# Kernel optimization log

Measured on AMD Instinct MI355X. Metric: run time of the kernel, lower is better.

The kernel has to match this reference:

```python
import jax, jax.numpy as jnp
import numpy as np

GRID = 32


def setup_inputs() -> dict:
    key = jax.random.key(0)
    k1, k2, k3 = jax.random.split(key, 3)
    # points in [-0.5, 0.5] per the module's asserts
    x = jax.random.uniform(k1, (8, 3, 50000), minval=-0.5, maxval=0.5, dtype=jnp.float32)
    # prep = Conv2d(3, 16, kernel_size=1): weight [C,3], bias [C]
    W = jax.random.normal(k2, (16, 3), dtype=jnp.float32) * 0.1
    bias = jax.random.normal(k3, (16,), dtype=jnp.float32) * 0.1
    return {"x": x, "W": W, "bias": bias}


def reference(x, W, bias):
    G = GRID
    b, _, n = x.shape
    reshaped = (x + 0.5) * G - 0.5                      # [b,3,n]
    ind1 = jnp.clip(jnp.floor(reshaped), 0.0, G - 1)
    ind2 = jnp.clip(jnp.ceil(reshaped), 0.0, G - 1)
    # 8 corners, ordered (floor/ceil over x, then y, then z) to match original list
    corners = []
    for cx in (ind1, ind2):
        for cy in (ind1, ind2):
            for cz in (ind1, ind2):
                corners.append(jnp.stack([cx[:, 0], cy[:, 1], cz[:, 2]], axis=1))
    ind = jnp.stack(corners, axis=-1)                   # [b,3,n,8]
    res = reshaped[..., None] - ind                     # [b,3,n,8] residuals
    flat_idx = (ind[:, 0] * (G * G) + ind[:, 1] * G + ind[:, 2]).astype(jnp.int32)  # [b,n,8]
    flat_idx = jnp.clip(flat_idx, 0, G ** 3)            # mirrors indices.clamp_(0, G**3)
    dist = jnp.linalg.norm(res, axis=1)                 # [b,n,8]
    weight = (dist < 0.87).astype(res.dtype)            # [b,n,8] (detached in original)
    # prep: 1x1 conv over channel dim
    feat = jnp.einsum('bknp,ck->bcnp', res, W) + bias[None, :, None, None]  # [b,c,n,8]
    feat = feat * weight[:, None]                       # mask by ball weight
    c = feat.shape[1]
    feat_f = feat.reshape(b, c, n * 8)
    w_f = jnp.broadcast_to(weight[:, None], feat.shape).reshape(b, c, n * 8)
    i_f = flat_idx.reshape(b, n * 8)

    def scatter_one(f, w, idx):
        g = jnp.zeros((c, G ** 3), f.dtype).at[:, idx].add(f)
        cnt = jnp.zeros((c, G ** 3), f.dtype).at[:, idx].add(w)
        return g, cnt

    grid, count = jax.vmap(scatter_one)(feat_f, w_f, i_f)  # [b,c,G^3] each
    grid = grid / jnp.maximum(count, 1.0)
    return grid.reshape(b, c, G, G, G)
```

## Files before the change

kernel.cpp:

```cpp
#include <hip/hip_runtime.h>

#define G 32
#define G2 (G*G)
#define G3 (G*G*G)
#define NPTS 50000
#define NB 8
#define NC 16
#define NCHUNK_PER_B 49
#define NCHUNK (NB*NCHUNK_PER_B)
#define SUBCAP 1024

#define OFF_HIST    0
#define OFF_PAYLOAD 65536

__global__ __launch_bounds__(1024) void ge_bin(const float* __restrict__ x,
                                               int* __restrict__ hist,
                                               float4* __restrict__ payload) {
    __shared__ float4 sp[2048];
    __shared__ unsigned char spl[2048];
    __shared__ int h[G];
    __shared__ int offs[G + 1];

    const int tid = threadIdx.x;
    const int b   = blockIdx.y;
    const int c   = b * NCHUNK_PER_B + blockIdx.x;
    const int n   = blockIdx.x * 1024 + tid;
    const bool valid = n < NPTS;

    if (tid < G) h[tid] = 0;
    __syncthreads();

    float rx = 0.f, ry = 0.f, rz = 0.f, fr1 = 1.0f;
    int p1 = 0, p2 = 0, r1 = 0, r2 = 0;
    if (valid) {
        const float* xb = x + (size_t)b * 3 * NPTS;
        rx = (xb[n]          + 0.5f) * 32.0f - 0.5f;
        ry = (xb[NPTS + n]   + 0.5f) * 32.0f - 0.5f;
        rz = (xb[2*NPTS + n] + 0.5f) * 32.0f - 0.5f;
        p1 = (int)fminf(fmaxf(floorf(rx), 0.0f), 31.0f);
        p2 = (int)fminf(fmaxf(ceilf (rx), 0.0f), 31.0f);
        if (p1 == p2) {
            fr1 = 2.0f;
            r1 = atomicAdd(&h[p1], 1);
        } else {
            r1 = atomicAdd(&h[p1], 1);
            r2 = atomicAdd(&h[p2], 1);
        }
    }
    __syncthreads();

    if (tid == 0) {
        int run = 0;
        #pragma unroll
        for (int p = 0; p < G; ++p) { offs[p] = run; run += h[p]; }
        offs[G] = run;
    }
    __syncthreads();

    if (valid) {
        int e1 = offs[p1] + r1;
        sp[e1]  = make_float4(rx, ry, rz, fr1);
        spl[e1] = (unsigned char)p1;
        if (p1 != p2) {
            int e2 = offs[p2] + r2;
            sp[e2]  = make_float4(rx, ry, rz, 1.0f);
            spl[e2] = (unsigned char)p2;
        }
    }
    if (tid < G) hist[c * G + tid] = h[tid];
    __syncthreads();

    const int T = offs[G];
    float4* chunk_pl = payload + (size_t)c * G * SUBCAP;
    for (int e = tid; e < T; e += 1024) {
        int p = spl[e];
        chunk_pl[(size_t)p * SUBCAP + (e - offs[p])] = sp[e];
    }
}

__global__ __launch_bounds__(1024) void ge_accum(const float4* __restrict__ payload,
                                                 const int* __restrict__ hist,
                                                 const float* __restrict__ W,
                                                 const float* __restrict__ bias,
                                                 float* __restrict__ out) {
    __shared__ unsigned long long A[G2];
    const int tid = threadIdx.x;
    const int b = blockIdx.x >> 5;
    const int s = blockIdx.x & 31;
    const float fs = (float)s;

    A[tid] = 0ull;
    __syncthreads();

    const int wave = tid >> 6, lane = tid & 63;
    for (int blk = wave; blk < NCHUNK_PER_B; blk += 16) {
        const int cc  = b * NCHUNK_PER_B + blk;
        const int ec  = hist[cc * G + s];
        const float4* q = payload + ((size_t)cc * G + s) * SUBCAP;
        for (int i = lane; i < ec; i += 64) {
            float4 e = q[i];
            float dx = e.x - fs;
            float ry = e.y, rz = e.z;
            unsigned fri = (unsigned)e.w;

            float fy1 = fminf(fmaxf(floorf(ry), 0.0f), 31.0f);
            float fy2 = fminf(fmaxf(ceilf (ry), 0.0f), 31.0f);
            float fz1 = fminf(fmaxf(floorf(rz), 0.0f), 31.0f);
            float fz2 = fminf(fmaxf(ceilf (rz), 0.0f), 31.0f);
            float dy1 = ry - fy1, dy2 = ry - fy2;
            float dz1 = rz - fz1, dz2 = rz - fz2;

            unsigned ax  = (unsigned)((int)rintf(dx  * 2048.0f) + 2048) * fri;
            unsigned ay1 = (unsigned)((int)rintf(dy1 * 2048.0f) + 2048) * fri;
            unsigned ay2 = (unsigned)((int)rintf(dy2 * 2048.0f) + 2048) * fri;
            unsigned az1 = (unsigned)((int)rintf(dz1 * 2048.0f) + 2048) * fri;
            unsigned az2 = (unsigned)((int)rintf(dz2 * 2048.0f) + 2048) * fri;
            unsigned long long base = ((unsigned long long)fri << 57)
                                    | ((unsigned long long)ax  << 38);
            float dx2 = dx * dx;

            #pragma unroll
            for (int cy = 0; cy < 2; ++cy) {
                float iy = cy ? fy2 : fy1;
                float dy = cy ? dy2 : dy1;
                unsigned ay = cy ? ay2 : ay1;
                float dxy2 = dx2 + dy * dy;
                #pragma unroll
                for (int cz = 0; cz < 2; ++cz) {
                    float iz = cz ? fz2 : fz1;
                    float dz = cz ? dz2 : dz1;
                    float d2 = dxy2 + dz * dz;
                    if (d2 < 0.7569f) {
                        int cell = (int)iy * G + (int)iz;
                        unsigned az = cz ? az2 : az1;
                        atomicAdd(&A[cell],
                                  base | ((unsigned long long)ay << 19)
                                       | (unsigned long long)az);
                    }
                }
            }
        }
    }
    __syncthreads();

    const unsigned long long a = A[tid];
    const float cw = (float)(unsigned)(a >> 57);
    const float fxs = (float)(unsigned)((a >> 38) & 0x7FFFFull);
    const float fys = (float)(unsigned)((a >> 19) & 0x7FFFFull);
    const float fzs = (float)(unsigned)( a         & 0x7FFFFull);
    const float k = 1.0f / 2048.0f;
    const float sx = (fxs - 2048.0f * cw) * k;
    const float sy = (fys - 2048.0f * cw) * k;
    const float sz = (fzs - 2048.0f * cw) * k;
    const float inv = 1.0f / fmaxf(cw, 1.0f);

    float* ob = out + (size_t)b * NC * G3 + (size_t)s * G2 + tid;
    #pragma unroll
    for (int ch = 0; ch < NC; ++ch) {
        float v = W[ch * 3 + 0] * sx + W[ch * 3 + 1] * sy + W[ch * 3 + 2] * sz
                + cw * bias[ch];
        ob[(size_t)ch * G3] = v * inv;
    }
}

#define SEG 12288
#define QMAX SEG
__global__ __launch_bounds__(1024) void ge_fused(const float* __restrict__ x,
                                                 const float* __restrict__ W,
                                                 const float* __restrict__ bias,
                                                 float* __restrict__ out) {
    __shared__ float acc[G2][4];
    __shared__ int   q[QMAX];
    __shared__ int   qcount;
    const int b = blockIdx.x >> 5;
    const int s = blockIdx.x & 31;
    const float fs = (float)s;
    const int lane = threadIdx.x & 63;
    for (int i = threadIdx.x; i < G2 * 4; i += 1024) ((float*)acc)[i] = 0.0f;
    if (threadIdx.x == 0) qcount = 0;
    __syncthreads();
    const float* xb = x + (size_t)b * 3 * NPTS;
    for (int seg = 0; seg < NPTS; seg += SEG) {
        const int seg_end = (seg + SEG < NPTS) ? seg + SEG : NPTS;
        for (int base = seg; base < seg_end; base += 1024) {
            int n = base + threadIdx.x;
            bool pred = false; int tag = 0;
            if (n < seg_end) {
                float rx = (xb[n] + 0.5f) * 32.0f - 0.5f;
                int p1 = (int)fminf(fmaxf(floorf(rx), 0.0f), 31.0f);
                int p2 = (int)fminf(fmaxf(ceilf (rx), 0.0f), 31.0f);
                int reps = (p1 == s) + (p2 == s);
                pred = reps > 0;
                tag = n | (reps == 2 ? (int)0x80000000 : 0);
            }
            unsigned long long mask = __ballot(pred);
            int wcnt = __popcll(mask);
            if (wcnt) {
                int wbase = 0;
                if (lane == 0) wbase = atomicAdd(&qcount, wcnt);
                wbase = __shfl(wbase, 0);
                if (pred) q[wbase + __popcll(mask & ((1ULL << lane) - 1ULL))] = tag;
            }
        }
        __syncthreads();
        const int cnt = qcount;
        for (int i = threadIdx.x; i < cnt; i += 1024) {
            int e = q[i];
            int n = e & 0x7fffffff;
            float fr = (e < 0) ? 2.0f : 1.0f;
            float rx = (xb[n]          + 0.5f) * 32.0f - 0.5f;
            float ry = (xb[NPTS + n]   + 0.5f) * 32.0f - 0.5f;
            float rz = (xb[2*NPTS + n] + 0.5f) * 32.0f - 0.5f;
            float dx = rx - fs;
            float fy1 = fminf(fmaxf(floorf(ry), 0.0f), 31.0f);
            float fy2 = fminf(fmaxf(ceilf (ry), 0.0f), 31.0f);
            float fz1 = fminf(fmaxf(floorf(rz), 0.0f), 31.0f);
            float fz2 = fminf(fmaxf(ceilf (rz), 0.0f), 31.0f);
            #pragma unroll
            for (int cy = 0; cy < 2; ++cy) {
                float iy = cy ? fy2 : fy1;
                float dy = ry - iy;
                #pragma unroll
                for (int cz = 0; cz < 2; ++cz) {
                    float iz = cz ? fz2 : fz1;
                    float dz = rz - iz;
                    float d2 = dx * dx + dy * dy + dz * dz;
                    if (d2 < 0.7569f) {
                        int cell = (int)iy * G + (int)iz;
                        atomicAdd(&acc[cell][0], fr * dx);
                        atomicAdd(&acc[cell][1], fr * dy);
                        atomicAdd(&acc[cell][2], fr * dz);
                        atomicAdd(&acc[cell][3], fr);
                    }
                }
            }
        }
        __syncthreads();
        if (threadIdx.x == 0) qcount = 0;
        __syncthreads();
    }
    int cell = threadIdx.x;
    float sx = acc[cell][0], sy = acc[cell][1], sz = acc[cell][2], cnt = acc[cell][3];
    float inv = 1.0f / fmaxf(cnt, 1.0f);
    float* ob = out + (size_t)b * NC * G3 + (size_t)s * G2 + cell;
    #pragma unroll
    for (int c = 0; c < NC; ++c) {
        float v = W[c * 3 + 0] * sx + W[c * 3 + 1] * sy + W[c * 3 + 2] * sz
                + cnt * bias[c];
        ob[(size_t)c * G3] = v * inv;
    }
}

extern "C" void kernel_launch(void* const* d_in, const int* in_sizes, int n_in,
                              void* d_out, int out_size, void* d_ws, size_t ws_size,
                              hipStream_t stream) {
    const float* x    = (const float*)d_in[0];
    const float* W    = (const float*)d_in[1];
    const float* bias = (const float*)d_in[2];
    float* out = (float*)d_out;

    const size_t need = OFF_PAYLOAD + (size_t)NCHUNK * G * SUBCAP * sizeof(float4);
    if (ws_size >= need) {
        char* wsb = (char*)d_ws;
        int*    hist    = (int*)(wsb + OFF_HIST);
        float4* payload = (float4*)(wsb + OFF_PAYLOAD);

        ge_bin  <<<dim3(NCHUNK_PER_B, NB), 1024, 0, stream>>>(x, hist, payload);
        ge_accum<<<NB * G, 1024, 0, stream>>>(payload, hist, W, bias, out);
    } else {
        ge_fused<<<NB * G, 1024, 0, stream>>>(x, W, bias, out);
    }
}
```

Baseline: 22.06 us.

## Pack binned point payload into 64-bit records with precomputed corner masks

The binning kernel now computes the y/z floor/ceil indices, quantized residuals and the four-corner distance mask up front. It packs them into a single 64-bit record instead of a float4, and drops x-slabs where no corner passes the radius test. This halves the payload traffic between the two kernels and cuts the per-entry ALU work in the accumulate kernel to bit unpacking and masked atomics. The exchange is more work in the bin kernel and tighter bit-field packing, which must stay consistent with the accumulator's field layout.

```diff
diff --git a/kernel.cpp b/kernel.cpp
--- a/kernel.cpp
+++ b/kernel.cpp
@@ -13,10 +13,11 @@
 #define OFF_HIST    0
 #define OFF_PAYLOAD 65536
 
+
 __global__ __launch_bounds__(1024) void ge_bin(const float* __restrict__ x,
                                                int* __restrict__ hist,
-                                               float4* __restrict__ payload) {
-    __shared__ float4 sp[2048];
+                                               unsigned long long* __restrict__ payload) {
+    __shared__ unsigned long long sp[2048];
     __shared__ unsigned char spl[2048];
     __shared__ int h[G];
     __shared__ int offs[G + 1];
@@ -30,21 +31,72 @@
     if (tid < G) h[tid] = 0;
     __syncthreads();
 
-    float rx = 0.f, ry = 0.f, rz = 0.f, fr1 = 1.0f;
+    unsigned long long e1 = 0, e2 = 0;
     int p1 = 0, p2 = 0, r1 = 0, r2 = 0;
+    bool put1 = false, put2 = false;
+
     if (valid) {
         const float* xb = x + (size_t)b * 3 * NPTS;
-        rx = (xb[n]          + 0.5f) * 32.0f - 0.5f;
-        ry = (xb[NPTS + n]   + 0.5f) * 32.0f - 0.5f;
-        rz = (xb[2*NPTS + n] + 0.5f) * 32.0f - 0.5f;
+        float rx = (xb[n]          + 0.5f) * 32.0f - 0.5f;
+        float ry = (xb[NPTS + n]   + 0.5f) * 32.0f - 0.5f;
+        float rz = (xb[2*NPTS + n] + 0.5f) * 32.0f - 0.5f;
         p1 = (int)fminf(fmaxf(floorf(rx), 0.0f), 31.0f);
         p2 = (int)fminf(fmaxf(ceilf (rx), 0.0f), 31.0f);
-        if (p1 == p2) {
-            fr1 = 2.0f;
-            r1 = atomicAdd(&h[p1], 1);
-        } else {
-            r1 = atomicAdd(&h[p1], 1);
-            r2 = atomicAdd(&h[p2], 1);
+
+        float fy1 = fminf(fmaxf(floorf(ry), 0.0f), 31.0f);
+        float fy2 = fminf(fmaxf(ceilf (ry), 0.0f), 31.0f);
+        float fz1 = fminf(fmaxf(floorf(rz), 0.0f), 31.0f);
+        float fz2 = fminf(fmaxf(ceilf (rz), 0.0f), 31.0f);
+        float dy1 = ry - fy1, dy2 = ry - fy2;
+        float dz1 = rz - fz1, dz2 = rz - fz2;
+        float dy1s = dy1 * dy1, dy2s = dy2 * dy2;
+        float dz1s = dz1 * dz1, dz2s = dz2 * dz2;
+
+        int iy1 = (int)fy1, sy = (int)fy2 - iy1;
+        int iz1 = (int)fz1, sz = (int)fz2 - iz1;
+        int ay1 = (int)rintf(dy1 * 2048.0f) + 2048;
+        int az1 = (int)rintf(dz1 * 2048.0f) + 2048;
+        unsigned long long common =
+              ((unsigned long long)(unsigned)ay1 << 30)
+            | ((unsigned long long)(unsigned)az1 << 17)
+            | ((unsigned long long)(unsigned)iy1 << 12)
+            | ((unsigned long long)(unsigned)iz1 << 7)
+            | ((unsigned long long)(unsigned)sy  << 6)
+            | ((unsigned long long)(unsigned)sz  << 5);
+        unsigned fr1 = (p1 == p2) ? 2u : 1u;
+
+        {
+            float dx = rx - (float)p1;
+            float dx2 = dx * dx;
+            float a0 = dx2 + dy1s, a1 = dx2 + dy2s;
+            unsigned m = 0;
+            if (a0 + dz1s < 0.7569f) m |= 1u;
+            if (a0 + dz2s < 0.7569f) m |= 2u;
+            if (a1 + dz1s < 0.7569f) m |= 4u;
+            if (a1 + dz2s < 0.7569f) m |= 8u;
+            if (m) {
+                unsigned ax = (unsigned)((int)rintf(dx * 2048.0f) + 2048);
+                e1 = ((unsigned long long)ax << 43) | common
+                   | ((unsigned long long)(fr1 - 1u) << 4) | m;
+                put1 = true;
+                r1 = atomicAdd(&h[p1], 1);
+            }
+        }
+        if (p2 != p1) {
+            float dx = rx - (float)p2;
+            float dx2 = dx * dx;
+            float a0 = dx2 + dy1s, a1 = dx2 + dy2s;
+            unsigned m = 0;
+            if (a0 + dz1s < 0.7569f) m |= 1u;
+            if (a0 + dz2s < 0.7569f) m |= 2u;
+            if (a1 + dz1s < 0.7569f) m |= 4u;
+            if (a1 + dz2s < 0.7569f) m |= 8u;
+            if (m) {
+                unsigned ax = (unsigned)((int)rintf(dx * 2048.0f) + 2048);
+                e2 = ((unsigned long long)ax << 43) | common | m;
+                put2 = true;
+                r2 = atomicAdd(&h[p2], 1);
+            }
         }
     }
     __syncthreads();
@@ -57,28 +109,26 @@
     }
     __syncthreads();
 
-    if (valid) {
-        int e1 = offs[p1] + r1;
-        sp[e1]  = make_float4(rx, ry, rz, fr1);
-        spl[e1] = (unsigned char)p1;
-        if (p1 != p2) {
-            int e2 = offs[p2] + r2;
-            sp[e2]  = make_float4(rx, ry, rz, 1.0f);
-            spl[e2] = (unsigned char)p2;
-        }
+    if (put1) {
+        int i1 = offs[p1] + r1;
+        sp[i1] = e1; spl[i1] = (unsigned char)p1;
+    }
+    if (put2) {
+        int i2 = offs[p2] + r2;
+        sp[i2] = e2; spl[i2] = (unsigned char)p2;
     }
     if (tid < G) hist[c * G + tid] = h[tid];
     __syncthreads();
 
     const int T = offs[G];
-    float4* chunk_pl = payload + (size_t)c * G * SUBCAP;
+    unsigned long long* chunk_pl = payload + (size_t)c * G * SUBCAP;
     for (int e = tid; e < T; e += 1024) {
         int p = spl[e];
         chunk_pl[(size_t)p * SUBCAP + (e - offs[p])] = sp[e];
     }
 }
 
-__global__ __launch_bounds__(1024) void ge_accum(const float4* __restrict__ payload,
+__global__ __launch_bounds__(1024) void ge_accum(const unsigned long long* __restrict__ payload,
                                                  const int* __restrict__ hist,
                                                  const float* __restrict__ W,
                                                  const float* __restrict__ bias,
@@ -87,71 +137,54 @@
     const int tid = threadIdx.x;
     const int b = blockIdx.x >> 5;
     const int s = blockIdx.x & 31;
-    const float fs = (float)s;
 
     A[tid] = 0ull;
     __syncthreads();
 
     const int wave = tid >> 6, lane = tid & 63;
     for (int blk = wave; blk < NCHUNK_PER_B; blk += 16) {
-        const int cc  = b * NCHUNK_PER_B + blk;
-        const int ec  = hist[cc * G + s];
-        const float4* q = payload + ((size_t)cc * G + s) * SUBCAP;
+        const int cc = b * NCHUNK_PER_B + blk;
+        const int ec = hist[cc * G + s];
+        const unsigned long long* q = payload + ((size_t)cc * G + s) * SUBCAP;
         for (int i = lane; i < ec; i += 64) {
-            float4 e = q[i];
-            float dx = e.x - fs;
-            float ry = e.y, rz = e.z;
-            unsigned fri = (unsigned)e.w;
-
-            float fy1 = fminf(fmaxf(floorf(ry), 0.0f), 31.0f);
-            float fy2 = fminf(fmaxf(ceilf (ry), 0.0f), 31.0f);
-            float fz1 = fminf(fmaxf(floorf(rz), 0.0f), 31.0f);
-            float fz2 = fminf(fmaxf(ceilf (rz), 0.0f), 31.0f);
-            float dy1 = ry - fy1, dy2 = ry - fy2;
-            float dz1 = rz - fz1, dz2 = rz - fz2;
-
-            unsigned ax  = (unsigned)((int)rintf(dx  * 2048.0f) + 2048) * fri;
-            unsigned ay1 = (unsigned)((int)rintf(dy1 * 2048.0f) + 2048) * fri;
-            unsigned ay2 = (unsigned)((int)rintf(dy2 * 2048.0f) + 2048) * fri;
-            unsigned az1 = (unsigned)((int)rintf(dz1 * 2048.0f) + 2048) * fri;
-            unsigned az2 = (unsigned)((int)rintf(dz2 * 2048.0f) + 2048) * fri;
-            unsigned long long base = ((unsigned long long)fri << 57)
-                                    | ((unsigned long long)ax  << 38);
-            float dx2 = dx * dx;
-
-            #pragma unroll
-            for (int cy = 0; cy < 2; ++cy) {
-                float iy = cy ? fy2 : fy1;
-                float dy = cy ? dy2 : dy1;
-                unsigned ay = cy ? ay2 : ay1;
-                float dxy2 = dx2 + dy * dy;
-                #pragma unroll
-                for (int cz = 0; cz < 2; ++cz) {
-                    float iz = cz ? fz2 : fz1;
-                    float dz = cz ? dz2 : dz1;
-                    float d2 = dxy2 + dz * dz;
-                    if (d2 < 0.7569f) {
-                        int cell = (int)iy * G + (int)iz;
-                        unsigned az = cz ? az2 : az1;
-                        atomicAdd(&A[cell],
-                                  base | ((unsigned long long)ay << 19)
-                                       | (unsigned long long)az);
-                    }
-                }
-            }
+            unsigned long long e = q[i];
+            unsigned m   = (unsigned)e & 15u;
+            unsigned fr  = 1u + (((unsigned)e >> 4) & 1u);
+            int sz  = ((int)e >> 5) & 1;
+            int sy  = ((int)e >> 6) & 1;
+            int iz1 = ((int)e >> 7) & 31;
+            int iy1 = ((int)e >> 12) & 31;
+            unsigned az1 = (unsigned)(e >> 17) & 0x1FFFu;
+            unsigned ay1 = (unsigned)(e >> 30) & 0x1FFFu;
+            unsigned ax  = (unsigned)(e >> 43) & 0x1FFFu;
+
+            unsigned long long base = ((unsigned long long)fr << 57)
+                                    | ((unsigned long long)(ax * fr) << 38);
+            unsigned ayl = ay1 * fr, ayh = (ay1 - 2048u * sy) * fr;
+            unsigned azl = az1 * fr, azh = (az1 - 2048u * sz) * fr;
+            int cell = iy1 * G + iz1;
+
+            if (m & 1u) atomicAdd(&A[cell],
+                ((unsigned long long)ayl << 19) | azl | base);
+            if (m & 2u) atomicAdd(&A[cell + sz],
+                ((unsigned long long)ayl << 19) | azh | base);
+            if (m & 4u) atomicAdd(&A[cell + G * sy],
+                ((unsigned long long)ayh << 19) | azl | base);
+            if (m & 8u) atomicAdd(&A[cell + G * sy + sz],
+                ((unsigned long long)ayh << 19) | azh | base);
         }
     }
     __syncthreads();
 
     const unsigned long long a = A[tid];
-    const float cw = (float)(unsigned)(a >> 57);
+    const float cw  = (float)(unsigned)(a >> 57);
     const float fxs = (float)(unsigned)((a >> 38) & 0x7FFFFull);
     const float fys = (float)(unsigned)((a >> 19) & 0x7FFFFull);
     const float fzs = (float)(unsigned)( a         & 0x7FFFFull);
-    const float k = 1.0f / 2048.0f;
-    const float sx = (fxs - 2048.0f * cw) * k;
-    const float sy = (fys - 2048.0f * cw) * k;
-    const float sz = (fzs - 2048.0f * cw) * k;
+    const float kq = 1.0f / 2048.0f;
+    const float sx = (fxs - 2048.0f * cw) * kq;
+    const float sy = (fys - 2048.0f * cw) * kq;
+    const float sz = (fzs - 2048.0f * cw) * kq;
     const float inv = 1.0f / fmaxf(cw, 1.0f);
 
     float* ob = out + (size_t)b * NC * G3 + (size_t)s * G2 + tid;
@@ -259,11 +292,12 @@
     const float* bias = (const float*)d_in[2];
     float* out = (float*)d_out;
 
-    const size_t need = OFF_PAYLOAD + (size_t)NCHUNK * G * SUBCAP * sizeof(float4);
+    const size_t need = OFF_PAYLOAD
+                      + (size_t)NCHUNK * G * SUBCAP * sizeof(unsigned long long);
     if (ws_size >= need) {
         char* wsb = (char*)d_ws;
-        int*    hist    = (int*)(wsb + OFF_HIST);
-        float4* payload = (float4*)(wsb + OFF_PAYLOAD);
+        int* hist = (int*)(wsb + OFF_HIST);
+        unsigned long long* payload = (unsigned long long*)(wsb + OFF_PAYLOAD);
 
         ge_bin  <<<dim3(NCHUNK_PER_B, NB), 1024, 0, stream>>>(x, hist, payload);
         ge_accum<<<NB * G, 1024, 0, stream>>>(payload, hist, W, bias, out);
```

New measurement: 19.24 us. 1.15x faster.
